# Kernel optimization log

Measured on AMD Instinct MI355X. Metric: run time of the kernel, lower is better.

Reference implementation:

```python
import jax, jax.numpy as jnp
import numpy as np

B, N, DQ, DK, DV, H = 8, 1024, 512, 512, 512, 8
DH = DV // H  # 64


def setup_inputs() -> dict:
    key = jax.random.key(0)
    ks = jax.random.split(key, 12)
    Q = jax.random.normal(ks[0], (B, N, DQ), jnp.float32)
    K = jax.random.normal(ks[1], (B, N, DK), jnp.float32)
    U = jax.random.normal(ks[2], (H, N, N, B), jnp.float32) * 0.1  # additive bias, [H,Nq,Nk,B]
    mask = (jax.random.uniform(ks[3], (B, N)) < 0.9).astype(jnp.float32)
    w = 0.02
    return {
        'Q': Q, 'K': K, 'U': U, 'mask': mask,
        'Wq': jax.random.normal(ks[4], (DQ, DV), jnp.float32) * w,
        'bq': jnp.zeros((DV,), jnp.float32),
        'Wk': jax.random.normal(ks[5], (DK, DV), jnp.float32) * w,
        'bk': jnp.zeros((DV,), jnp.float32),
        'Wv': jax.random.normal(ks[6], (DK, DV), jnp.float32) * w,
        'bv': jnp.zeros((DV,), jnp.float32),
        'Wo': jax.random.normal(ks[7], (DV, DV), jnp.float32) * w,
        'bo': jnp.zeros((DV,), jnp.float32),
    }


def reference(Q, K, U, mask, Wq, bq, Wk, bk, Wv, bv, Wo, bo):
    m = mask[:, :, None]  # [B,N,1]
    q = (Q @ Wq + bq) * m  # [B,N,DV]
    k = (K @ Wk + bk) * m
    v = (K @ Wv + bv) * m
    # split heads: torch.cat(split(dh,2),0) is head-major -> [H,B,N,DH]
    qh = q.reshape(B, N, H, DH).transpose(2, 0, 1, 3)
    kh = k.reshape(B, N, H, DH).transpose(2, 0, 1, 3)
    vh = v.reshape(B, N, H, DH).transpose(2, 0, 1, 3)
    # U.transpose(1,3).transpose(-1,-2).reshape(H*B,N,N) == transpose(U,(0,3,1,2))
    bias = jnp.transpose(U, (0, 3, 1, 2))  # [H,B,Nq,Nk]
    scores = jnp.einsum('hbid,hbjd->hbij', qh, kh) / np.sqrt(DV) + bias
    # custom double-masked softmax (max taken over unmasked scores, faithfully)
    max_elem = jnp.max(scores, axis=3, keepdims=True)
    m1 = mask[None, :, :, None]  # [1,B,Nq,1]
    m2 = mask[None, :, None, :]  # [1,B,1,Nk]
    num = jnp.exp((scores - max_elem) * m1 * m2) * m1 * m2
    A = num / (jnp.sum(num, axis=3, keepdims=True) + 1e-16)
    o = qh + jnp.einsum('hbij,hbjd->hbid', A, vh)  # residual, [H,B,N,DH]
    O = o.transpose(1, 2, 0, 3).reshape(B, N, DV)  # merge heads
    O = O + jax.nn.relu((O @ Wo + bo) * m)
    return O
```

## Files before the change

### kernel.cpp

```cpp
#include <hip/hip_runtime.h>

#define B_   8
#define N_   1024
#define D_   512
#define H_   8
#define DH_  64
#define SCALE_ 0.044194173824159216f
#define LOG2E_ 1.4426950408889634f

typedef __attribute__((ext_vector_type(8))) short bf16x8;
typedef __attribute__((ext_vector_type(4))) float f32x4;
typedef __attribute__((ext_vector_type(8))) unsigned short us8;
typedef __attribute__((ext_vector_type(4))) unsigned int u32x4;

__device__ __forceinline__ unsigned short f2bf(float f) {
  unsigned u = __builtin_bit_cast(unsigned, f);
  u += 0x7fffu + ((u >> 16) & 1u);
  return (unsigned short)(u >> 16);
}
__device__ __forceinline__ float bf2f(unsigned short h) {
  unsigned u = ((unsigned)h) << 16;
  return __builtin_bit_cast(float, u);
}
__device__ __forceinline__ void gl_lds16(const void* g, void* l) {
  __builtin_amdgcn_global_load_lds(
      (const __attribute__((address_space(1))) unsigned int*)g,
      (__attribute__((address_space(3))) unsigned int*)l, 16, 0, 0);
}
__device__ __forceinline__ unsigned cvt_pk_bf16(float lo, float hi) {
  unsigned r;
  asm("v_cvt_pk_bf16_f32 %0, %1, %2" : "=v"(r) : "v"(lo), "v"(hi));
  return r;
}
#define MFMA16(a, b, c) __builtin_amdgcn_mfma_f32_16x16x32_bf16((a), (b), (c), 0, 0, 0)
#define SCHED_PIN() __builtin_amdgcn_sched_barrier(0)

__global__ void prep_w(const float* __restrict__ Wq, const float* __restrict__ Wk,
                       const float* __restrict__ Wv, const float* __restrict__ Wo,
                       unsigned short* __restrict__ WT) {
  int idx = blockIdx.x * 256 + threadIdx.x;
  int mat = idx >> 18;
  int rem = idx & 0x3FFFF;
  int k = rem >> 9, n = rem & 511;
  const float* W = (mat == 0) ? Wq : (mat == 1) ? Wk : (mat == 2) ? Wv : Wo;
  float v = W[(size_t)k * 512 + n];
  int kmap = (k & ~63) | ((k & 63) ^ ((n & 7) << 3));
  WT[(size_t)mat * 262144 + (size_t)n * 512 + kmap] = f2bf(v);
}

#define GEMM_BODY(A, W, bias, EPILOGUE)                                          \
  __shared__ unsigned short Alds[2][128][72];                                    \
  __shared__ unsigned short Blds[2][128 * 64];                                   \
  const int t = threadIdx.x, w = t >> 6, l = t & 63;                             \
  const int wr = w >> 1, wc = w & 1;                                             \
  const int lm = l & 15, lg = l >> 4;                                            \
  const int bm = blockIdx.x >> 2, bn = blockIdx.x & 3;                           \
  f32x4 acc[4][4];                                                               \
  _Pragma("unroll") for (int mt = 0; mt < 4; ++mt)                               \
  _Pragma("unroll") for (int nt = 0; nt < 4; ++nt)                               \
      acc[mt][nt] = f32x4{0.f, 0.f, 0.f, 0.f};                                   \
  float4 areg[8];                                                                \
  auto loadA = [&](int kt) {                                                     \
    _Pragma("unroll") for (int p = 0; p < 8; ++p) {                              \
      int row = (t >> 4) + p * 16, col = (t & 15) * 4;                           \
      areg[p] = *(const float4*)&A[((size_t)(bm * 128 + row)) * 512 + kt * 64 + col]; \
    }                                                                            \
  };                                                                             \
  auto issueB = [&](int kt, int sb) {                                            \
    _Pragma("unroll") for (int p = 0; p < 4; ++p) {                              \
      int chunk = w * 4 + p;                                                     \
      int row = chunk * 8 + (l >> 3), gc = kt * 64 + (l & 7) * 8;                \
      gl_lds16(&W[((size_t)(bn * 128 + row)) * 512 + gc],                        \
               &Blds[sb][chunk * 512 + l * 8]);                                  \
    }                                                                            \
  };                                                                             \
  auto writeA = [&](int sb) {                                                    \
    _Pragma("unroll") for (int p = 0; p < 8; ++p) {                              \
      int row = (t >> 4) + p * 16, col = (t & 15) * 4;                           \
      float4 v = areg[p];                                                        \
      uint2 d;                                                                   \
      d.x = (unsigned)f2bf(v.x) | ((unsigned)f2bf(v.y) << 16);                   \
      d.y = (unsigned)f2bf(v.z) | ((unsigned)f2bf(v.w) << 16);                   \
      *(uint2*)&Alds[sb][row][col] = d;                                          \
    }                                                                            \
  };                                                                             \
  loadA(0); issueB(0, 0); writeA(0);                                             \
  __syncthreads();                                                               \
  int buf = 0;                                                                   \
  for (int kt = 0; kt < 8; ++kt) {                                               \
    if (kt + 1 < 8) { loadA(kt + 1); issueB(kt + 1, buf ^ 1); }                  \
    _Pragma("unroll") for (int kk = 0; kk < 2; ++kk) {                           \
      bf16x8 af[4], bfv[4];                                                      \
      _Pragma("unroll") for (int mt = 0; mt < 4; ++mt)                           \
        af[mt] = *(const bf16x8*)&Alds[buf][wr * 64 + mt * 16 + lm][kk * 32 + lg * 8]; \
      _Pragma("unroll") for (int nt = 0; nt < 4; ++nt) {                         \
        int rr = wc * 64 + nt * 16 + lm;                                         \
        int c = (kk * 32 + lg * 8) ^ ((rr & 7) << 3);                            \
        bfv[nt] = *(const bf16x8*)&Blds[buf][rr * 64 + c];                       \
      }                                                                          \
      _Pragma("unroll") for (int mt = 0; mt < 4; ++mt)                           \
      _Pragma("unroll") for (int nt = 0; nt < 4; ++nt)                           \
          acc[mt][nt] = MFMA16(af[mt], bfv[nt], acc[mt][nt]);                    \
    }                                                                            \
    if (kt + 1 < 8) writeA(buf ^ 1);                                             \
    __syncthreads();                                                             \
    buf ^= 1;                                                                    \
  }                                                                              \
  _Pragma("unroll") for (int mt = 0; mt < 4; ++mt)                               \
  _Pragma("unroll") for (int nt = 0; nt < 4; ++nt) {                             \
    int gn = bn * 128 + wc * 64 + nt * 16 + lm;                                  \
    float bv_ = bias[gn];                                                        \
    _Pragma("unroll") for (int e = 0; e < 4; ++e) {                              \
      int gm = bm * 128 + wr * 64 + mt * 16 + lg * 4 + e;                        \
      float v = acc[mt][nt][e] + bv_;                                            \
      size_t off = (size_t)gm * 512 + gn;                                        \
      EPILOGUE                                                                   \
    }                                                                            \
  }

__global__ __launch_bounds__(256, 2) void gemm_proj3(
    const float* __restrict__ Q, const float* __restrict__ K,
    const unsigned short* __restrict__ WT,
    const float* __restrict__ bq, const float* __restrict__ bk,
    const float* __restrict__ bv, const float* __restrict__ mask,
    unsigned short* __restrict__ qb, unsigned short* __restrict__ kb,
    unsigned short* __restrict__ vtmp) {
  const int mat = blockIdx.y;
  const float* A = (mat == 0) ? Q : K;
  const unsigned short* W = WT + (size_t)mat * 262144;
  const float* bias = (mat == 0) ? bq : (mat == 1) ? bk : bv;
  unsigned short* outp = (mat == 0) ? qb : (mat == 1) ? kb : vtmp;
  GEMM_BODY(A, W, bias, { outp[off] = f2bf(v * mask[gm]); })
}

__global__ __launch_bounds__(256, 2) void gemm_final(
    const float* __restrict__ A, const unsigned short* __restrict__ W,
    const float* __restrict__ bias, const float* __restrict__ mask,
    const float* __restrict__ resid, float* __restrict__ outp) {
  GEMM_BODY(A, W, bias, { outp[off] = resid[off] + fmaxf(v, 0.f) * mask[gm]; })
}

__global__ void vtrans_kernel(const unsigned short* __restrict__ vtmp,
                              unsigned short* __restrict__ vT) {
  __shared__ unsigned short T[64][72];
  int b = blockIdx.x, ntile = blockIdx.y, dtile = blockIdx.z;
  int n0 = ntile * 64, d0 = dtile * 64;
  int t = threadIdx.x;
#pragma unroll
  for (int p = 0; p < 2; ++p) {
    int r = (t >> 3) + p * 32;
    int c = (t & 7) * 8;
    *(us8*)&T[r][c] = *(const us8*)&vtmp[((size_t)(b * N_ + n0 + r)) * D_ + d0 + c];
  }
  __syncthreads();
#pragma unroll
  for (int p = 0; p < 2; ++p) {
    int r = (t >> 3) + p * 32;
    int c = (t & 7) * 8;
    us8 v;
#pragma unroll
    for (int e = 0; e < 8; ++e) v[e] = T[c + e][r];
    *(us8*)&vT[((size_t)(b * D_ + d0 + r)) * N_ + n0 + c] = v;
  }
}

__global__ __launch_bounds__(512, 4) void attn_kernel(
    const unsigned short* __restrict__ qb, const unsigned short* __restrict__ kb,
    const unsigned short* __restrict__ vT, const float* __restrict__ U,
    const float* __restrict__ mask, float* __restrict__ O32) {
  __shared__ float Ulds[2 * 4096];
  __shared__ float Plds[8][16 * 36];
  const int t = threadIdx.x, w = t >> 6, l = t & 63;
  const int bid = (int)blockIdx.x;
  const int h = bid & 7;
  const int i0 = (bid >> 3) * 16;
  const int b = w;
  const int lm = l & 15, lg = l >> 4;

  const int sti = t >> 5, stj = t & 31;
  const float* Ug = U + (((size_t)h * N_ + i0 + sti) * N_ + stj) * B_;
  const int pbase = sti * 256 + ((stj ^ (sti >> 2)) & 31) * 8;
  const int bh0 = (stj >> 2) & 1;
  const int rot = stj & 3;

  auto rot4 = [&](float4 v) {
    if (rot & 1) v = float4{v.y, v.x, v.w, v.z};
    if (rot & 2) v = float4{v.z, v.w, v.x, v.y};
    return v;
  };
  auto stageLoad = [&](float4& a, float4& c, int jt) {
    const float* g = Ug + (size_t)jt * 256;
    a = *(const float4*)(g);
    c = *(const float4*)(g + 4);
  };
  auto stageWrite = [&](const float4& a, const float4& c, int sb) {
    *(float4*)&Ulds[sb * 4096 + pbase + (0 ^ bh0) * 4] = rot4(a);
    *(float4*)&Ulds[sb * 4096 + pbase + (1 ^ bh0) * 4] = rot4(c);
  };

  const int ubase = ((lm ^ lg) * 8) + (((w >> 2) ^ ((lm >> 2) & 1)) * 4) + ((w & 3) ^ (lm & 3)) + lg * 1024;

  const unsigned short* Kb = kb + (size_t)b * N_ * D_ + h * DH_ + lg * 8;
  const unsigned short* Vb = vT + ((size_t)b * D_ + h * DH_ + lm) * N_ + lg * 8;
  const float* Mb = mask + b * N_ + lm;

  bf16x8 qf[2];
#pragma unroll
  for (int kt = 0; kt < 2; ++kt)
    qf[kt] = *(const bf16x8*)&qb[((size_t)b * N_ + i0 + lm) * D_ + h * DH_ + kt * 32 + lg * 8];

  f32x4 acc[4];
#pragma unroll
  for (int nt = 0; nt < 4; ++nt) acc[nt] = f32x4{0.f, 0.f, 0.f, 0.f};
  float lrun[4] = {0.f, 0.f, 0.f, 0.f};

  bf16x8 kf[2][2], vf[4];
  auto loadK = [&](int jt) {
#pragma unroll
    for (int j2 = 0; j2 < 2; ++j2)
#pragma unroll
      for (int kt = 0; kt < 2; ++kt)
        kf[j2][kt] = *(const bf16x8*)&Kb[(size_t)(jt * 32 + j2 * 16 + lm) * D_ + kt * 32];
  };

  float4 uaA, ubA, uaB, ubB;
  float mj0, mj1, mjn0, mjn1;

  stageLoad(uaA, ubA, 0);
  stageWrite(uaA, ubA, 0);
  stageLoad(uaB, ubB, 1);
  loadK(0);
  mj0 = Mb[0]; mj1 = Mb[16];
  SCHED_PIN();
  asm volatile("s_waitcnt lgkmcnt(0)");
  __builtin_amdgcn_sched_barrier(0);
  __builtin_amdgcn_s_barrier();

#define ATTN_BODY(T, BUFR, SWa, SWb, SLa, SLb)                                   \
  {                                                                              \
    _Pragma("unroll") for (int nt = 0; nt < 4; ++nt)                             \
      vf[nt] = *(const bf16x8*)&Vb[(size_t)nt * 16 * N_ + (T) * 32];             \
    SCHED_PIN();                                                                 \
    f32x4 S0 = f32x4{0.f, 0.f, 0.f, 0.f}, S1 = f32x4{0.f, 0.f, 0.f, 0.f};       \
    _Pragma("unroll") for (int kt = 0; kt < 2; ++kt) {                           \
      S0 = MFMA16(qf[kt], kf[0][kt], S0);                                        \
      S1 = MFMA16(qf[kt], kf[1][kt], S1);                                        \
    }                                                                            \
    if ((T) + 1 < 32) {                                                          \
      loadK((T) + 1);                                                            \
      mjn0 = Mb[((T) + 1) * 32]; mjn1 = Mb[((T) + 1) * 32 + 16];                 \
    }                                                                            \
    SCHED_PIN();                                                                 \
    _Pragma("unroll") for (int e = 0; e < 4; ++e) {                              \
      float u0 = Ulds[(BUFR) * 4096 + e * 256 + ubase];                          \
      float u1 = Ulds[(BUFR) * 4096 + e * 256 + 128 + ubase];                    \
      float s0 = S0[e] * SCALE_ + u0;                                            \
      float s1 = S1[e] * SCALE_ + u1;                                            \
      float p0 = (mj0 != 0.f) ? exp2f(s0 * LOG2E_) : 0.f;                        \
      float p1 = (mj1 != 0.f) ? exp2f(s1 * LOG2E_) : 0.f;                        \
      lrun[e] += p0 + p1;                                                        \
      Plds[w][(lg * 4 + e) * 36 + lm] = p0;                                      \
      Plds[w][(lg * 4 + e) * 36 + lm + 16] = p1;                                 \
    }                                                                            \
    float4 pa0 = *(const float4*)&Plds[w][lm * 36 + lg * 8];                     \
    float4 pa1 = *(const float4*)&Plds[w][lm * 36 + lg * 8 + 4];                 \
    u32x4 pk;                                                                    \
    pk[0] = cvt_pk_bf16(pa0.x, pa0.y);                                           \
    pk[1] = cvt_pk_bf16(pa0.z, pa0.w);                                           \
    pk[2] = cvt_pk_bf16(pa1.x, pa1.y);                                           \
    pk[3] = cvt_pk_bf16(pa1.z, pa1.w);                                           \
    bf16x8 paf = __builtin_bit_cast(bf16x8, pk);                                 \
    _Pragma("unroll") for (int nt = 0; nt < 4; ++nt)                             \
      acc[nt] = MFMA16(paf, vf[nt], acc[nt]);                                    \
    if ((T) + 1 < 32) stageWrite(SWa, SWb, (BUFR) ^ 1);                          \
    if ((T) + 2 < 32) stageLoad(SLa, SLb, (T) + 2);                              \
    mj0 = mjn0; mj1 = mjn1;                                                      \
    SCHED_PIN();                                                                 \
    asm volatile("s_waitcnt lgkmcnt(0)");                                        \
    __builtin_amdgcn_sched_barrier(0);                                           \
    __builtin_amdgcn_s_barrier();                                                \
  }

  for (int jt = 0; jt < 32; jt += 2) {
    ATTN_BODY(jt,     0, uaB, ubB, uaA, ubA)
    ATTN_BODY(jt + 1, 1, uaA, ubA, uaB, ubB)
  }
#undef ATTN_BODY

#pragma unroll
  for (int e = 0; e < 4; ++e) {
    float lv = lrun[e];
    lv += __shfl_xor(lv, 1);
    lv += __shfl_xor(lv, 2);
    lv += __shfl_xor(lv, 4);
    lv += __shfl_xor(lv, 8);
    int gi = i0 + lg * 4 + e;
    float mi = mask[b * N_ + gi];
    float rD = 1.f / (lv + 1e-16f);
#pragma unroll
    for (int nt = 0; nt < 4; ++nt) {
      size_t off = ((size_t)b * N_ + gi) * D_ + h * DH_ + lm + nt * 16;
      float qv = bf2f(qb[off]);
      O32[off] = mi * (qv + acc[nt][e] * rD);
    }
  }
}

extern "C" void kernel_launch(void* const* d_in, const int* in_sizes, int n_in,
                              void* d_out, int out_size, void* d_ws, size_t ws_size,
                              hipStream_t stream) {
  const float* Q    = (const float*)d_in[0];
  const float* K    = (const float*)d_in[1];
  const float* U    = (const float*)d_in[2];
  const float* mask = (const float*)d_in[3];
  const float* Wq   = (const float*)d_in[4];
  const float* bq   = (const float*)d_in[5];
  const float* Wk   = (const float*)d_in[6];
  const float* bk   = (const float*)d_in[7];
  const float* Wv   = (const float*)d_in[8];
  const float* bv   = (const float*)d_in[9];
  const float* Wo   = (const float*)d_in[10];
  const float* bo   = (const float*)d_in[11];
  float* out = (float*)d_out;

  char* ws = (char*)d_ws;
  unsigned short* WT   = (unsigned short*)ws;
  unsigned short* qb   = (unsigned short*)(ws + (2llu << 20));
  unsigned short* kb   = (unsigned short*)(ws + (10llu << 20));
  unsigned short* vtmp = (unsigned short*)(ws + (18llu << 20));
  unsigned short* vTb  = (unsigned short*)(ws + (26llu << 20));
  float* O32           = (float*)(ws + (34llu << 20));

  prep_w<<<4096, 256, 0, stream>>>(Wq, Wk, Wv, Wo, WT);
  gemm_proj3<<<dim3(256, 3), 256, 0, stream>>>(Q, K, WT, bq, bk, bv, mask, qb, kb, vtmp);
  vtrans_kernel<<<dim3(8, 16, 8), 256, 0, stream>>>(vtmp, vTb);
  attn_kernel<<<512, 512, 0, stream>>>(qb, kb, vTb, U, mask, O32);
  gemm_final<<<256, 256, 0, stream>>>(O32, WT + 3 * 262144, bo, mask, O32, out);
}
```

Before: 232.1 us.

## Redistribute softmax work so U is read directly into registers, dropping LDS staging

The attention kernel stops staging the [H,N,N,B] bias tile through a double-buffered LDS area with rotations. Each wave now writes its raw QK scores to LDS. After a barrier, each thread handles one (i,j) pair across all 8 batches, using a contiguous 8-float U load held in registers and a per-key 8-bit mask word built by a new prep kernel. Probabilities go back through LDS to the MFMA layout, and row sums are reduced across threads via LDS at the end. This removes the U LDS transpose but adds a second block barrier per tile and more LDS traffic.

```diff
diff --git a/kernel.cpp b/kernel.cpp
--- a/kernel.cpp
+++ b/kernel.cpp
@@ -46,6 +46,14 @@
   float v = W[(size_t)k * 512 + n];
   int kmap = (k & ~63) | ((k & 63) ^ ((n & 7) << 3));
   WT[(size_t)mat * 262144 + (size_t)n * 512 + kmap] = f2bf(v);
+}
+
+__global__ void prep_mask(const float* __restrict__ mask, unsigned* __restrict__ mbits) {
+  int j = blockIdx.x * 256 + threadIdx.x;
+  unsigned r = 0;
+#pragma unroll
+  for (int bb = 0; bb < 8; ++bb) r |= (mask[bb * N_ + j] != 0.f ? 1u : 0u) << bb;
+  mbits[j] = r;
 }
 
 #define GEMM_BODY(A, W, bias, EPILOGUE)                                          \
@@ -167,52 +175,37 @@
 __global__ __launch_bounds__(512, 4) void attn_kernel(
     const unsigned short* __restrict__ qb, const unsigned short* __restrict__ kb,
     const unsigned short* __restrict__ vT, const float* __restrict__ U,
-    const float* __restrict__ mask, float* __restrict__ O32) {
-  __shared__ float Ulds[2 * 4096];
-  __shared__ float Plds[8][16 * 36];
+    const unsigned* __restrict__ mbits, const float* __restrict__ mask,
+    float* __restrict__ O32) {
+  __shared__ float Slds[8 * 544];
+  __shared__ float Plds[8 * 576];
+  __shared__ float Dlds[128];
   const int t = threadIdx.x, w = t >> 6, l = t & 63;
   const int bid = (int)blockIdx.x;
   const int h = bid & 7;
   const int i0 = (bid >> 3) * 16;
-  const int b = w;
   const int lm = l & 15, lg = l >> 4;
-
-  const int sti = t >> 5, stj = t & 31;
-  const float* Ug = U + (((size_t)h * N_ + i0 + sti) * N_ + stj) * B_;
-  const int pbase = sti * 256 + ((stj ^ (sti >> 2)) & 31) * 8;
-  const int bh0 = (stj >> 2) & 1;
-  const int rot = stj & 3;
-
-  auto rot4 = [&](float4 v) {
-    if (rot & 1) v = float4{v.y, v.x, v.w, v.z};
-    if (rot & 2) v = float4{v.z, v.w, v.x, v.y};
-    return v;
-  };
-  auto stageLoad = [&](float4& a, float4& c, int jt) {
-    const float* g = Ug + (size_t)jt * 256;
-    a = *(const float4*)(g);
-    c = *(const float4*)(g + 4);
-  };
-  auto stageWrite = [&](const float4& a, const float4& c, int sb) {
-    *(float4*)&Ulds[sb * 4096 + pbase + (0 ^ bh0) * 4] = rot4(a);
-    *(float4*)&Ulds[sb * 4096 + pbase + (1 ^ bh0) * 4] = rot4(c);
-  };
-
-  const int ubase = ((lm ^ lg) * 8) + (((w >> 2) ^ ((lm >> 2) & 1)) * 4) + ((w & 3) ^ (lm & 3)) + lg * 1024;
-
-  const unsigned short* Kb = kb + (size_t)b * N_ * D_ + h * DH_ + lg * 8;
-  const unsigned short* Vb = vT + ((size_t)b * D_ + h * DH_ + lm) * N_ + lg * 8;
-  const float* Mb = mask + b * N_ + lm;
+  const int ti = t >> 5, tj = t & 31;
+
+  const float* Ug = U + (((size_t)h * N_ + i0 + ti) * N_ + tj) * B_;
+  const unsigned short* Kb = kb + (size_t)w * N_ * D_ + h * DH_ + lg * 8;
+  const unsigned short* Vb = vT + ((size_t)w * D_ + h * DH_ + lm) * N_ + lg * 8;
+
+  const int swr0 = w * 544 + lm * 17 + lg * 4;
+  const int swr1 = w * 544 + (lm + 16) * 17 + lg * 4;
+  const int srd  = tj * 17 + ti;
+  const int pwr  = ti * 36 + tj;
+  const int prd  = w * 576 + lm * 36 + lg * 8;
 
   bf16x8 qf[2];
 #pragma unroll
   for (int kt = 0; kt < 2; ++kt)
-    qf[kt] = *(const bf16x8*)&qb[((size_t)b * N_ + i0 + lm) * D_ + h * DH_ + kt * 32 + lg * 8];
+    qf[kt] = *(const bf16x8*)&qb[((size_t)w * N_ + i0 + lm) * D_ + h * DH_ + kt * 32 + lg * 8];
 
   f32x4 acc[4];
 #pragma unroll
   for (int nt = 0; nt < 4; ++nt) acc[nt] = f32x4{0.f, 0.f, 0.f, 0.f};
-  float lrun[4] = {0.f, 0.f, 0.f, 0.f};
+  float lrun[8] = {0.f, 0.f, 0.f, 0.f, 0.f, 0.f, 0.f, 0.f};
 
   bf16x8 kf[2][2], vf[4];
   auto loadK = [&](int jt) {
@@ -222,48 +215,65 @@
       for (int kt = 0; kt < 2; ++kt)
         kf[j2][kt] = *(const bf16x8*)&Kb[(size_t)(jt * 32 + j2 * 16 + lm) * D_ + kt * 32];
   };
-
-  float4 uaA, ubA, uaB, ubB;
-  float mj0, mj1, mjn0, mjn1;
-
-  stageLoad(uaA, ubA, 0);
-  stageWrite(uaA, ubA, 0);
-  stageLoad(uaB, ubB, 1);
+  auto loadV = [&](int jt) {
+#pragma unroll
+    for (int nt = 0; nt < 4; ++nt)
+      vf[nt] = *(const bf16x8*)&Vb[(size_t)nt * 16 * N_ + jt * 32];
+  };
+
+  float4 uA0, uA1, uB0, uB1;
+  unsigned mbA, mbB;
+
   loadK(0);
-  mj0 = Mb[0]; mj1 = Mb[16];
-  SCHED_PIN();
-  asm volatile("s_waitcnt lgkmcnt(0)");
-  __builtin_amdgcn_sched_barrier(0);
-  __builtin_amdgcn_s_barrier();
-
-#define ATTN_BODY(T, BUFR, SWa, SWb, SLa, SLb)                                   \
+  loadV(0);
+  uA0 = *(const float4*)(Ug);
+  uA1 = *(const float4*)(Ug + 4);
+  mbA = mbits[tj];
+
+#define ATTN_BODY(T, PF, UC0, UC1, MBC, UN0, UN1, MBN)                           \
   {                                                                              \
-    _Pragma("unroll") for (int nt = 0; nt < 4; ++nt)                             \
-      vf[nt] = *(const bf16x8*)&Vb[(size_t)nt * 16 * N_ + (T) * 32];             \
-    SCHED_PIN();                                                                 \
+                                                       \
     f32x4 S0 = f32x4{0.f, 0.f, 0.f, 0.f}, S1 = f32x4{0.f, 0.f, 0.f, 0.f};       \
     _Pragma("unroll") for (int kt = 0; kt < 2; ++kt) {                           \
       S0 = MFMA16(qf[kt], kf[0][kt], S0);                                        \
       S1 = MFMA16(qf[kt], kf[1][kt], S1);                                        \
     }                                                                            \
-    if ((T) + 1 < 32) {                                                          \
-      loadK((T) + 1);                                                            \
-      mjn0 = Mb[((T) + 1) * 32]; mjn1 = Mb[((T) + 1) * 32 + 16];                 \
-    }                                                                            \
+    if (PF) loadK((T) + 1);                                                      \
     SCHED_PIN();                                                                 \
     _Pragma("unroll") for (int e = 0; e < 4; ++e) {                              \
-      float u0 = Ulds[(BUFR) * 4096 + e * 256 + ubase];                          \
-      float u1 = Ulds[(BUFR) * 4096 + e * 256 + 128 + ubase];                    \
-      float s0 = S0[e] * SCALE_ + u0;                                            \
-      float s1 = S1[e] * SCALE_ + u1;                                            \
-      float p0 = (mj0 != 0.f) ? exp2f(s0 * LOG2E_) : 0.f;                        \
-      float p1 = (mj1 != 0.f) ? exp2f(s1 * LOG2E_) : 0.f;                        \
-      lrun[e] += p0 + p1;                                                        \
-      Plds[w][(lg * 4 + e) * 36 + lm] = p0;                                      \
-      Plds[w][(lg * 4 + e) * 36 + lm + 16] = p1;                                 \
-    }                                                                            \
-    float4 pa0 = *(const float4*)&Plds[w][lm * 36 + lg * 8];                     \
-    float4 pa1 = *(const float4*)&Plds[w][lm * 36 + lg * 8 + 4];                 \
+      Slds[swr0 + e] = S0[e];                                                    \
+      Slds[swr1 + e] = S1[e];                                                    \
+    }                                                                            \
+    SCHED_PIN();                                                                 \
+    asm volatile("s_waitcnt lgkmcnt(0)" ::: "memory");                           \
+    SCHED_PIN();                                                                 \
+    __builtin_amdgcn_s_barrier();                                                \
+    SCHED_PIN();                                                                 \
+                   \
+    if (PF) {                                                                    \
+      UN0 = *(const float4*)(Ug + ((T) + 1) * 256);                              \
+      UN1 = *(const float4*)(Ug + ((T) + 1) * 256 + 4);                          \
+      MBN = mbits[((T) + 1) * 32 + tj];                                          \
+    }                                                                            \
+    SCHED_PIN();                                                                 \
+    float uu[8];                                                                 \
+    uu[0] = UC0.x; uu[1] = UC0.y; uu[2] = UC0.z; uu[3] = UC0.w;                  \
+    uu[4] = UC1.x; uu[5] = UC1.y; uu[6] = UC1.z; uu[7] = UC1.w;                  \
+    _Pragma("unroll") for (int b = 0; b < 8; ++b) {                              \
+      float sv = Slds[b * 544 + srd];                                            \
+      float s = sv * SCALE_ + uu[b];                                             \
+      float p = ((MBC >> b) & 1) ? exp2f(s * LOG2E_) : 0.f;                      \
+      lrun[b] += p;                                                              \
+      Plds[b * 576 + pwr] = p;                                                   \
+    }                                                                            \
+    SCHED_PIN();                                                                 \
+    asm volatile("s_waitcnt lgkmcnt(0)" ::: "memory");                           \
+    SCHED_PIN();                                                                 \
+    __builtin_amdgcn_s_barrier();                                                \
+    SCHED_PIN();                                                                 \
+                                 \
+    float4 pa0 = *(const float4*)&Plds[prd];                                     \
+    float4 pa1 = *(const float4*)&Plds[prd + 4];                                 \
     u32x4 pk;                                                                    \
     pk[0] = cvt_pk_bf16(pa0.x, pa0.y);                                           \
     pk[1] = cvt_pk_bf16(pa0.z, pa0.w);                                           \
@@ -272,34 +282,41 @@
     bf16x8 paf = __builtin_bit_cast(bf16x8, pk);                                 \
     _Pragma("unroll") for (int nt = 0; nt < 4; ++nt)                             \
       acc[nt] = MFMA16(paf, vf[nt], acc[nt]);                                    \
-    if ((T) + 1 < 32) stageWrite(SWa, SWb, (BUFR) ^ 1);                          \
-    if ((T) + 2 < 32) stageLoad(SLa, SLb, (T) + 2);                              \
-    mj0 = mjn0; mj1 = mjn1;                                                      \
-    SCHED_PIN();                                                                 \
-    asm volatile("s_waitcnt lgkmcnt(0)");                                        \
-    __builtin_amdgcn_sched_barrier(0);                                           \
-    __builtin_amdgcn_s_barrier();                                                \
-  }
-
-  for (int jt = 0; jt < 32; jt += 2) {
-    ATTN_BODY(jt,     0, uaB, ubB, uaA, ubA)
-    ATTN_BODY(jt + 1, 1, uaA, ubA, uaB, ubB)
-  }
+    if (PF) loadV((T) + 1);                                                      \
+  }
+
+  for (int jt = 0; jt < 30; jt += 2) {
+    ATTN_BODY(jt,     1, uA0, uA1, mbA, uB0, uB1, mbB)
+    ATTN_BODY(jt + 1, 1, uB0, uB1, mbB, uA0, uA1, mbA)
+  }
+  ATTN_BODY(30, 1, uA0, uA1, mbA, uB0, uB1, mbB)
+  ATTN_BODY(31, 0, uB0, uB1, mbB, uA0, uA1, mbA)
 #undef ATTN_BODY
 
 #pragma unroll
-  for (int e = 0; e < 4; ++e) {
-    float lv = lrun[e];
+  for (int b = 0; b < 8; ++b) {
+    float lv = lrun[b];
     lv += __shfl_xor(lv, 1);
     lv += __shfl_xor(lv, 2);
     lv += __shfl_xor(lv, 4);
     lv += __shfl_xor(lv, 8);
+    lv += __shfl_xor(lv, 16);
+    lrun[b] = lv;
+  }
+  if (tj == 0) {
+#pragma unroll
+    for (int b = 0; b < 8; ++b) Dlds[b * 16 + ti] = lrun[b];
+  }
+  __syncthreads();
+
+#pragma unroll
+  for (int e = 0; e < 4; ++e) {
     int gi = i0 + lg * 4 + e;
-    float mi = mask[b * N_ + gi];
-    float rD = 1.f / (lv + 1e-16f);
+    float mi = mask[w * N_ + gi];
+    float rD = 1.f / (Dlds[w * 16 + lg * 4 + e] + 1e-16f);
 #pragma unroll
     for (int nt = 0; nt < 4; ++nt) {
-      size_t off = ((size_t)b * N_ + gi) * D_ + h * DH_ + lm + nt * 16;
+      size_t off = ((size_t)w * N_ + gi) * D_ + h * DH_ + lm + nt * 16;
       float qv = bf2f(qb[off]);
       O32[off] = mi * (qv + acc[nt][e] * rD);
     }
@@ -330,10 +347,12 @@
   unsigned short* vtmp = (unsigned short*)(ws + (18llu << 20));
   unsigned short* vTb  = (unsigned short*)(ws + (26llu << 20));
   float* O32           = (float*)(ws + (34llu << 20));
+  unsigned* mbits      = (unsigned*)(ws + (50llu << 20));
 
   prep_w<<<4096, 256, 0, stream>>>(Wq, Wk, Wv, Wo, WT);
+  prep_mask<<<4, 256, 0, stream>>>(mask, mbits);
   gemm_proj3<<<dim3(256, 3), 256, 0, stream>>>(Q, K, WT, bq, bk, bv, mask, qb, kb, vtmp);
   vtrans_kernel<<<dim3(8, 16, 8), 256, 0, stream>>>(vtmp, vTb);
-  attn_kernel<<<512, 512, 0, stream>>>(qb, kb, vTb, U, mask, O32);
+  attn_kernel<<<512, 512, 0, stream>>>(qb, kb, vTb, U, mbits, mask, O32);
   gemm_final<<<256, 256, 0, stream>>>(O32, WT + 3 * 262144, bo, mask, O32, out);
 }
```

Measured after the change: 231.9 us. No clear change (-0.1%).
